# Kernel optimization log

Measured on AMD Instinct MI355X. Metric: run time of the kernel, lower is better.

The kernel has to match this reference:

```python
import jax, jax.numpy as jnp
import numpy as np

N, L, S, D, K, H, G = 512, 1024, 3, 128, 4, 32, 64


def setup_inputs() -> dict:
    key = jax.random.key(0)
    ks = jax.random.split(key, 12)
    f = lambda i, shape, s=1.0: jax.random.normal(ks[i], shape, dtype=jnp.float32) * s
    return dict(
        scores=f(0, (N, 1, L, S)),
        veh_repr=f(1, (N, 1, D)),
        cust_repr=f(2, (N, L, D)),
        edge_emb=f(3, (N, 1, L, D)),
        expert_w1=f(4, (K, S, H), 0.3),
        expert_b1=jnp.zeros((K, H), jnp.float32),
        expert_w2=f(5, (K, H, 1), 0.3),
        expert_b2=jnp.zeros((K, 1), jnp.float32),
        sit_w1=f(6, (2 * D, G), 0.05),
        sit_b1=jnp.zeros((G,), jnp.float32),
        sit_w2=f(7, (G, K), 0.1),
        sit_b2=jnp.zeros((K,), jnp.float32),
        cand_w=f(8, (S, K), 0.3),
        cand_b=jnp.zeros((K,), jnp.float32),
        edge_w=f(9, (D, K), 0.05),
        gate_balance=jnp.zeros((), jnp.float32),
    )


def reference(scores, veh_repr, cust_repr, edge_emb,
              expert_w1, expert_b1, expert_w2, expert_b2,
              sit_w1, sit_b1, sit_w2, sit_b2,
              cand_w, cand_b, edge_w, gate_balance):
    # Inference mode: no gate noise, no dropout (identity at eval).
    # Situation gating: vehicle repr + graph context -> (N,1,K) logits
    graph_ctx = cust_repr.mean(axis=1, keepdims=True)              # (N,1,D)
    sit_in = jnp.concatenate([veh_repr, graph_ctx], axis=-1)       # (N,1,2D)
    hg = jax.nn.gelu(sit_in @ sit_w1 + sit_b1, approximate=False)  # (N,1,G)
    sit_logits = hg @ sit_w2 + sit_b2                              # (N,1,K)

    # Candidate-level gating from raw scores + edge embeddings
    cand_logits = scores @ cand_w + cand_b + edge_emb @ edge_w     # (N,1,L,K)

    alpha = jax.nn.sigmoid(gate_balance)
    gate_logits = alpha * sit_logits[:, :, None, :] + (1.0 - alpha) * cand_logits
    gate_w = jax.nn.softmax(gate_logits, axis=-1)                  # (N,1,L,K)

    # Per-expert tiny MLP over the S score channels
    h = jax.nn.gelu(jnp.einsum('nqls,ksh->nqlkh', scores, expert_w1) + expert_b1,
                    approximate=False)                             # (N,1,L,K,H)
    expert_out = jnp.einsum('nqlkh,kho->nqlko', h, expert_w2)[..., 0] + expert_b2[:, 0]

    fused = (gate_w * expert_out).sum(axis=-1)                     # (N,1,L)
    return fused
```

## Files before the change

kernel.cpp:

```cpp
#include <hip/hip_runtime.h>

#define NN 512
#define LL 1024
#define SS 3
#define DD 128
#define KK 4
#define HH 32
#define GG 64
#define NL (NN * LL)

__device__ __forceinline__ float fast_gelu(float x) {
    const float c0 = 0.7978845608028654f;
    const float c1 = 0.7978845608028654f * 0.044715f;
    float u = x * x;
    float y = x * fmaf(c1, u, c0);
    float e = __expf(2.0f * y);
    float r = __builtin_amdgcn_rcpf(e + 1.0f);
    float t = fmaf(-2.0f, r, 1.0f);
    return 0.5f * x * (1.0f + t);
}

__global__ __launch_bounds__(256) void k_sit(
    const float* __restrict__ veh, const float* __restrict__ cust,
    const float* __restrict__ w1, const float* __restrict__ b1,
    const float* __restrict__ w2, const float* __restrict__ b2,
    float* __restrict__ sit_out)
{
    __shared__ float4 red[256];
    __shared__ float sin_[2 * DD];
    __shared__ float hg[GG];
    const int n = blockIdx.x;
    const int t = threadIdx.x;
    const int c = t & 31, rs = t >> 5;
    const float4* cp = (const float4*)(cust + (size_t)n * LL * DD);

    float4 a0 = make_float4(0.f, 0.f, 0.f, 0.f), a1 = a0, a2 = a0, a3 = a0;
    for (int l = rs; l < LL; l += 32) {
        float4 v0 = cp[(l     ) * 32 + c];
        float4 v1 = cp[(l +  8) * 32 + c];
        float4 v2 = cp[(l + 16) * 32 + c];
        float4 v3 = cp[(l + 24) * 32 + c];
        a0.x += v0.x; a0.y += v0.y; a0.z += v0.z; a0.w += v0.w;
        a1.x += v1.x; a1.y += v1.y; a1.z += v1.z; a1.w += v1.w;
        a2.x += v2.x; a2.y += v2.y; a2.z += v2.z; a2.w += v2.w;
        a3.x += v3.x; a3.y += v3.y; a3.z += v3.z; a3.w += v3.w;
    }
    a0.x += a1.x + a2.x + a3.x;
    a0.y += a1.y + a2.y + a3.y;
    a0.z += a1.z + a2.z + a3.z;
    a0.w += a1.w + a2.w + a3.w;
    red[t] = a0;
    __syncthreads();

    if (t < 32) {
        float4 s = red[t];
        #pragma unroll
        for (int i = 1; i < 8; i++) {
            float4 v = red[i * 32 + t];
            s.x += v.x; s.y += v.y; s.z += v.z; s.w += v.w;
        }
        const float inv = 1.0f / (float)LL;
        sin_[DD + 4 * t + 0] = s.x * inv;
        sin_[DD + 4 * t + 1] = s.y * inv;
        sin_[DD + 4 * t + 2] = s.z * inv;
        sin_[DD + 4 * t + 3] = s.w * inv;
        float4 vv = ((const float4*)(veh + (size_t)n * DD))[t];
        sin_[4 * t + 0] = vv.x; sin_[4 * t + 1] = vv.y;
        sin_[4 * t + 2] = vv.z; sin_[4 * t + 3] = vv.w;
    }
    __syncthreads();

    if (t < GG) {
        float a = b1[t];
        #pragma unroll 8
        for (int i = 0; i < 2 * DD; i++)
            a = fmaf(sin_[i], w1[i * GG + t], a);
        hg[t] = fast_gelu(a);
    }
    __syncthreads();

    if (t < KK) {
        float a = b2[t];
        #pragma unroll
        for (int g = 0; g < GG; g++)
            a = fmaf(hg[g], w2[g * KK + t], a);
        sit_out[n * KK + t] = a;
    }
}

__global__ __launch_bounds__(256) void k_fuse(
    const float* __restrict__ scores, const float* __restrict__ edge,
    const float* __restrict__ sit,
    const float* __restrict__ ew1, const float* __restrict__ eb1,
    const float* __restrict__ ew2, const float* __restrict__ eb2,
    const float* __restrict__ cand_w, const float* __restrict__ cand_b,
    const float* __restrict__ edge_w, const float* __restrict__ gbp,
    float* __restrict__ out)
{
    const int lane = threadIdx.x & 63;
    const int r = lane & 31;
    const int wave = (blockIdx.x * blockDim.x + threadIdx.x) >> 6;
    const int gi0 = wave * 2 + (lane >> 5);
    const int stride = ((gridDim.x * blockDim.x) >> 6) * 2;

    const int ko = r & 3;
    const int jg = r >> 2;
    const bool kb0 = (r & 1) != 0;
    const bool kb1 = (r & 2) != 0;

    const float4* ew4 = (const float4*)edge_w;
    const float4 wqa = ew4[4 * r + 0];
    const float4 wqb = ew4[4 * r + 1];
    const float4 wqc = ew4[4 * r + 2];
    const float4 wqd = ew4[4 * r + 3];
    const float cw0 = cand_w[0 * KK + ko];
    const float cw1 = cand_w[1 * KK + ko];
    const float cw2 = cand_w[2 * KK + ko];
    const float cb  = cand_b[ko];
    const float4* w1f = (const float4*)ew1;
    const float4 w1a = w1f[(ko * SS + 0) * (HH / 4) + jg];
    const float4 w1b = w1f[(ko * SS + 1) * (HH / 4) + jg];
    const float4 w1c = w1f[(ko * SS + 2) * (HH / 4) + jg];
    const float4 b1v = ((const float4*)eb1)[ko * (HH / 4) + jg];
    const float4 w2v = ((const float4*)ew2)[ko * (HH / 4) + jg];
    const float b2o = eb2[ko];
    const float gbv = gbp[0];
    const float alpha = 1.0f / (1.0f + __expf(-gbv));
    const float onema = 1.0f - alpha;

    for (int e = gi0; e < NL; e += stride) {
        const float4 ev = *(const float4*)(edge + (size_t)e * DD + r * 4);
        float p0 = ev.x * wqa.x; p0 = fmaf(ev.y, wqb.x, p0); p0 = fmaf(ev.z, wqc.x, p0); p0 = fmaf(ev.w, wqd.x, p0);
        float p1 = ev.x * wqa.y; p1 = fmaf(ev.y, wqb.y, p1); p1 = fmaf(ev.z, wqc.y, p1); p1 = fmaf(ev.w, wqd.y, p1);
        float p2 = ev.x * wqa.z; p2 = fmaf(ev.y, wqb.z, p2); p2 = fmaf(ev.z, wqc.z, p2); p2 = fmaf(ev.w, wqd.z, p2);
        float p3 = ev.x * wqa.w; p3 = fmaf(ev.y, wqb.w, p3); p3 = fmaf(ev.z, wqc.w, p3); p3 = fmaf(ev.w, wqd.w, p3);
        p0 += __shfl_xor(p0, 1); p1 += __shfl_xor(p1, 1); p2 += __shfl_xor(p2, 1); p3 += __shfl_xor(p3, 1);
        p0 += __shfl_xor(p0, 2); p1 += __shfl_xor(p1, 2); p2 += __shfl_xor(p2, 2); p3 += __shfl_xor(p3, 2);
        float qa = kb0 ? p1 : p0;
        float qb = kb0 ? p3 : p2;
        float q  = kb1 ? qb : qa;
        q += __shfl_xor(q, 4); q += __shfl_xor(q, 8); q += __shfl_xor(q, 16);

        const float s0 = scores[(size_t)e * 3 + 0];
        const float s1 = scores[(size_t)e * 3 + 1];
        const float s2 = scores[(size_t)e * 3 + 2];

        float cand = fmaf(s0, cw0, fmaf(s1, cw1, fmaf(s2, cw2, cb))) + q;

        const float4 sl = *(const float4*)(sit + (e >> 10) * 4);
        float sa = kb0 ? sl.y : sl.x;
        float sb = kb0 ? sl.w : sl.z;
        float so = kb1 ? sb : sa;
        float gl = fmaf(alpha, so, onema * cand);

        float m = gl;
        m = fmaxf(m, __shfl_xor(m, 1));
        m = fmaxf(m, __shfl_xor(m, 2));
        float ex = __expf(gl - m);
        float se = ex;
        se += __shfl_xor(se, 1);
        se += __shfl_xor(se, 2);
        float gw = ex * __builtin_amdgcn_rcpf(se);

        float acc;
        {
            float z, h;
            z = fmaf(s0, w1a.x, fmaf(s1, w1b.x, fmaf(s2, w1c.x, b1v.x))); h = fast_gelu(z); acc = h * w2v.x;
            z = fmaf(s0, w1a.y, fmaf(s1, w1b.y, fmaf(s2, w1c.y, b1v.y))); h = fast_gelu(z); acc = fmaf(h, w2v.y, acc);
            z = fmaf(s0, w1a.z, fmaf(s1, w1b.z, fmaf(s2, w1c.z, b1v.z))); h = fast_gelu(z); acc = fmaf(h, w2v.z, acc);
            z = fmaf(s0, w1a.w, fmaf(s1, w1b.w, fmaf(s2, w1c.w, b1v.w))); h = fast_gelu(z); acc = fmaf(h, w2v.w, acc);
        }
        acc += __shfl_xor(acc, 4); acc += __shfl_xor(acc, 8); acc += __shfl_xor(acc, 16);

        float tk = gw * (acc + b2o);
        tk += __shfl_xor(tk, 1);
        tk += __shfl_xor(tk, 2);
        if (r == 0) out[e] = tk;
    }
}

extern "C" void kernel_launch(void* const* d_in, const int* in_sizes, int n_in,
                              void* d_out, int out_size, void* d_ws, size_t ws_size,
                              hipStream_t stream)
{
    const float* scores = (const float*)d_in[0];
    const float* veh    = (const float*)d_in[1];
    const float* cust   = (const float*)d_in[2];
    const float* edge   = (const float*)d_in[3];
    const float* ew1    = (const float*)d_in[4];
    const float* eb1    = (const float*)d_in[5];
    const float* ew2    = (const float*)d_in[6];
    const float* eb2    = (const float*)d_in[7];
    const float* sw1    = (const float*)d_in[8];
    const float* sb1    = (const float*)d_in[9];
    const float* sw2    = (const float*)d_in[10];
    const float* sb2    = (const float*)d_in[11];
    const float* cw     = (const float*)d_in[12];
    const float* cb     = (const float*)d_in[13];
    const float* egw    = (const float*)d_in[14];
    const float* gb     = (const float*)d_in[15];
    float* out = (float*)d_out;
    float* sit = (float*)d_ws;

    hipLaunchKernelGGL(k_sit, dim3(NN), dim3(256), 0, stream,
                       veh, cust, sw1, sb1, sw2, sb2, sit);
    hipLaunchKernelGGL(k_fuse, dim3(2048), dim3(256), 0, stream,
                       scores, edge, sit, ew1, eb1, ew2, eb2, cw, cb, egw, gb, out);
}
```

Before: 593.0 us.

## Fuse situation gating and candidate fusion into one per-row kernel

Merges the two kernels into a single kernel with one 512-thread block per batch row. Each block first reduces cust_repr and runs the situation MLP into shared memory, then processes that row's 1024 candidates. The sit logit and bias are folded into a per-thread constant. This removes a launch and the workspace round trip, but each block must finish the cust reduction before it can start the edge stream, so some overlap is lost and the grid shrinks to 512 blocks.

```diff
diff --git a/kernel.cpp b/kernel.cpp
--- a/kernel.cpp
+++ b/kernel.cpp
@@ -7,7 +7,6 @@
 #define KK 4
 #define HH 32
 #define GG 64
-#define NL (NN * LL)
 
 __device__ __forceinline__ float fast_gelu(float x) {
     const float c0 = 0.7978845608028654f;
@@ -20,94 +19,31 @@
     return 0.5f * x * (1.0f + t);
 }
 
-__global__ __launch_bounds__(256) void k_sit(
-    const float* __restrict__ veh, const float* __restrict__ cust,
-    const float* __restrict__ w1, const float* __restrict__ b1,
-    const float* __restrict__ w2, const float* __restrict__ b2,
-    float* __restrict__ sit_out)
-{
-    __shared__ float4 red[256];
-    __shared__ float sin_[2 * DD];
-    __shared__ float hg[GG];
-    const int n = blockIdx.x;
-    const int t = threadIdx.x;
-    const int c = t & 31, rs = t >> 5;
-    const float4* cp = (const float4*)(cust + (size_t)n * LL * DD);
-
-    float4 a0 = make_float4(0.f, 0.f, 0.f, 0.f), a1 = a0, a2 = a0, a3 = a0;
-    for (int l = rs; l < LL; l += 32) {
-        float4 v0 = cp[(l     ) * 32 + c];
-        float4 v1 = cp[(l +  8) * 32 + c];
-        float4 v2 = cp[(l + 16) * 32 + c];
-        float4 v3 = cp[(l + 24) * 32 + c];
-        a0.x += v0.x; a0.y += v0.y; a0.z += v0.z; a0.w += v0.w;
-        a1.x += v1.x; a1.y += v1.y; a1.z += v1.z; a1.w += v1.w;
-        a2.x += v2.x; a2.y += v2.y; a2.z += v2.z; a2.w += v2.w;
-        a3.x += v3.x; a3.y += v3.y; a3.z += v3.z; a3.w += v3.w;
-    }
-    a0.x += a1.x + a2.x + a3.x;
-    a0.y += a1.y + a2.y + a3.y;
-    a0.z += a1.z + a2.z + a3.z;
-    a0.w += a1.w + a2.w + a3.w;
-    red[t] = a0;
-    __syncthreads();
-
-    if (t < 32) {
-        float4 s = red[t];
-        #pragma unroll
-        for (int i = 1; i < 8; i++) {
-            float4 v = red[i * 32 + t];
-            s.x += v.x; s.y += v.y; s.z += v.z; s.w += v.w;
-        }
-        const float inv = 1.0f / (float)LL;
-        sin_[DD + 4 * t + 0] = s.x * inv;
-        sin_[DD + 4 * t + 1] = s.y * inv;
-        sin_[DD + 4 * t + 2] = s.z * inv;
-        sin_[DD + 4 * t + 3] = s.w * inv;
-        float4 vv = ((const float4*)(veh + (size_t)n * DD))[t];
-        sin_[4 * t + 0] = vv.x; sin_[4 * t + 1] = vv.y;
-        sin_[4 * t + 2] = vv.z; sin_[4 * t + 3] = vv.w;
-    }
-    __syncthreads();
-
-    if (t < GG) {
-        float a = b1[t];
-        #pragma unroll 8
-        for (int i = 0; i < 2 * DD; i++)
-            a = fmaf(sin_[i], w1[i * GG + t], a);
-        hg[t] = fast_gelu(a);
-    }
-    __syncthreads();
-
-    if (t < KK) {
-        float a = b2[t];
-        #pragma unroll
-        for (int g = 0; g < GG; g++)
-            a = fmaf(hg[g], w2[g * KK + t], a);
-        sit_out[n * KK + t] = a;
-    }
-}
-
-__global__ __launch_bounds__(256) void k_fuse(
-    const float* __restrict__ scores, const float* __restrict__ edge,
-    const float* __restrict__ sit,
+__global__ __launch_bounds__(512, 4) void k_all(
+    const float* __restrict__ scores, const float* __restrict__ veh,
+    const float* __restrict__ cust, const float* __restrict__ edge,
     const float* __restrict__ ew1, const float* __restrict__ eb1,
     const float* __restrict__ ew2, const float* __restrict__ eb2,
+    const float* __restrict__ sw1, const float* __restrict__ sb1,
+    const float* __restrict__ sw2, const float* __restrict__ sb2,
     const float* __restrict__ cand_w, const float* __restrict__ cand_b,
     const float* __restrict__ edge_w, const float* __restrict__ gbp,
     float* __restrict__ out)
 {
-    const int lane = threadIdx.x & 63;
+    __shared__ float4 red[512];
+    __shared__ float sin_[2 * DD];
+    __shared__ float hg[GG];
+    __shared__ float slds[KK];
+
+    const int n = blockIdx.x;
+    const int t = threadIdx.x;
+    const int lane = t & 63;
     const int r = lane & 31;
-    const int wave = (blockIdx.x * blockDim.x + threadIdx.x) >> 6;
-    const int gi0 = wave * 2 + (lane >> 5);
-    const int stride = ((gridDim.x * blockDim.x) >> 6) * 2;
 
     const int ko = r & 3;
     const int jg = r >> 2;
     const bool kb0 = (r & 1) != 0;
     const bool kb1 = (r & 2) != 0;
-
     const float4* ew4 = (const float4*)edge_w;
     const float4 wqa = ew4[4 * r + 0];
     const float4 wqb = ew4[4 * r + 1];
@@ -128,8 +64,78 @@
     const float alpha = 1.0f / (1.0f + __expf(-gbv));
     const float onema = 1.0f - alpha;
 
-    for (int e = gi0; e < NL; e += stride) {
-        const float4 ev = *(const float4*)(edge + (size_t)e * DD + r * 4);
+    const int c = t & 31;
+    const int rs = t >> 5;
+    const float4* cp = (const float4*)(cust + (size_t)n * LL * DD);
+    float4 a0 = make_float4(0.f, 0.f, 0.f, 0.f), a1 = a0, a2 = a0, a3 = a0;
+    #pragma unroll 4
+    for (int i = 0; i < 16; ++i) {
+        float4 v0 = cp[(rs + 16 * i      ) * 32 + c];
+        float4 v1 = cp[(rs + 16 * i + 256) * 32 + c];
+        float4 v2 = cp[(rs + 16 * i + 512) * 32 + c];
+        float4 v3 = cp[(rs + 16 * i + 768) * 32 + c];
+        a0.x += v0.x; a0.y += v0.y; a0.z += v0.z; a0.w += v0.w;
+        a1.x += v1.x; a1.y += v1.y; a1.z += v1.z; a1.w += v1.w;
+        a2.x += v2.x; a2.y += v2.y; a2.z += v2.z; a2.w += v2.w;
+        a3.x += v3.x; a3.y += v3.y; a3.z += v3.z; a3.w += v3.w;
+    }
+    a0.x += a1.x + a2.x + a3.x;
+    a0.y += a1.y + a2.y + a3.y;
+    a0.z += a1.z + a2.z + a3.z;
+    a0.w += a1.w + a2.w + a3.w;
+    red[t] = a0;
+    __syncthreads();
+
+    if (t < 32) {
+        float4 s = red[t];
+        #pragma unroll
+        for (int i = 1; i < 16; i++) {
+            float4 v = red[i * 32 + t];
+            s.x += v.x; s.y += v.y; s.z += v.z; s.w += v.w;
+        }
+        const float inv = 1.0f / (float)LL;
+        sin_[DD + 4 * t + 0] = s.x * inv;
+        sin_[DD + 4 * t + 1] = s.y * inv;
+        sin_[DD + 4 * t + 2] = s.z * inv;
+        sin_[DD + 4 * t + 3] = s.w * inv;
+        float4 vv = ((const float4*)(veh + (size_t)n * DD))[t];
+        sin_[4 * t + 0] = vv.x; sin_[4 * t + 1] = vv.y;
+        sin_[4 * t + 2] = vv.z; sin_[4 * t + 3] = vv.w;
+    }
+    __syncthreads();
+
+    if (t < GG) {
+        float a = sb1[t];
+        #pragma unroll 8
+        for (int i = 0; i < 2 * DD; i++)
+            a = fmaf(sin_[i], sw1[i * GG + t], a);
+        hg[t] = fast_gelu(a);
+    }
+    __syncthreads();
+    if (t < KK) {
+        float a = sb2[t];
+        #pragma unroll
+        for (int g = 0; g < GG; g++)
+            a = fmaf(hg[g], sw2[g * KK + t], a);
+        slds[t] = a;
+    }
+    __syncthreads();
+
+    const float sl0 = slds[0], sl1 = slds[1], sl2 = slds[2], sl3 = slds[3];
+    float sa_ = kb0 ? sl1 : sl0;
+    float sb_ = kb0 ? sl3 : sl2;
+    float so  = kb1 ? sb_ : sa_;
+    const float sbase = fmaf(alpha, so, onema * cb);
+
+    const int w = t >> 6;
+    const int half = lane >> 5;
+    const float* sc_base = scores + (size_t)n * LL * SS;
+    const float* ed_base = edge + (size_t)n * LL * DD;
+    float* out_base = out + (size_t)n * LL;
+
+    for (int i = 0; i < 64; ++i) {
+        const int el = w * 2 + half + i * 16;
+        const float4 ev = *(const float4*)(ed_base + (size_t)el * DD + r * 4);
         float p0 = ev.x * wqa.x; p0 = fmaf(ev.y, wqb.x, p0); p0 = fmaf(ev.z, wqc.x, p0); p0 = fmaf(ev.w, wqd.x, p0);
         float p1 = ev.x * wqa.y; p1 = fmaf(ev.y, wqb.y, p1); p1 = fmaf(ev.z, wqc.y, p1); p1 = fmaf(ev.w, wqd.y, p1);
         float p2 = ev.x * wqa.z; p2 = fmaf(ev.y, wqb.z, p2); p2 = fmaf(ev.z, wqc.z, p2); p2 = fmaf(ev.w, wqd.z, p2);
@@ -141,17 +147,12 @@
         float q  = kb1 ? qb : qa;
         q += __shfl_xor(q, 4); q += __shfl_xor(q, 8); q += __shfl_xor(q, 16);
 
-        const float s0 = scores[(size_t)e * 3 + 0];
-        const float s1 = scores[(size_t)e * 3 + 1];
-        const float s2 = scores[(size_t)e * 3 + 2];
-
-        float cand = fmaf(s0, cw0, fmaf(s1, cw1, fmaf(s2, cw2, cb))) + q;
-
-        const float4 sl = *(const float4*)(sit + (e >> 10) * 4);
-        float sa = kb0 ? sl.y : sl.x;
-        float sb = kb0 ? sl.w : sl.z;
-        float so = kb1 ? sb : sa;
-        float gl = fmaf(alpha, so, onema * cand);
+        const float s0 = sc_base[el * 3 + 0];
+        const float s1 = sc_base[el * 3 + 1];
+        const float s2 = sc_base[el * 3 + 2];
+
+        const float sdot = fmaf(s0, cw0, fmaf(s1, cw1, s2 * cw2));
+        const float gl = fmaf(onema, sdot + q, sbase);
 
         float m = gl;
         m = fmaxf(m, __shfl_xor(m, 1));
@@ -175,7 +176,7 @@
         float tk = gw * (acc + b2o);
         tk += __shfl_xor(tk, 1);
         tk += __shfl_xor(tk, 2);
-        if (r == 0) out[e] = tk;
+        if (r == 0) out_base[el] = tk;
     }
 }
 
@@ -200,10 +201,8 @@
     const float* egw    = (const float*)d_in[14];
     const float* gb     = (const float*)d_in[15];
     float* out = (float*)d_out;
-    float* sit = (float*)d_ws;
-
-    hipLaunchKernelGGL(k_sit, dim3(NN), dim3(256), 0, stream,
-                       veh, cust, sw1, sb1, sw2, sb2, sit);
-    hipLaunchKernelGGL(k_fuse, dim3(2048), dim3(256), 0, stream,
-                       scores, edge, sit, ew1, eb1, ew2, eb2, cw, cb, egw, gb, out);
+
+    hipLaunchKernelGGL(k_all, dim3(NN), dim3(512), 0, stream,
+                       scores, veh, cust, edge, ew1, eb1, ew2, eb2,
+                       sw1, sb1, sw2, sb2, cw, cb, egw, gb, out);
 }
```

After: 577.7 us. 1.03x faster.
